# Optimization experiments

Hardware: AMD Instinct MI355X
Metric: run time of the kernel (lower is better)

The kernel has to match this reference:

```python
import jax, jax.numpy as jnp
import numpy as np
from jax import lax

K, E, HID, NH, L = 512, 256, 512, 8, 2
N, S1, S2, C, U, V, W = 2, 8, 9, 3, 8, 8, 8
S = S1 + S2 - 1  # 16, matches sum(cfg['seq_length']) - 1


def setup_inputs() -> dict:
    key = jax.random.key(0)
    ks = iter(jax.random.split(key, 40))
    g = lambda shape, s=0.02: jax.random.normal(next(ks), shape, jnp.float32) * s
    inp = {
        'code': jax.random.randint(next(ks), (N, S1, C, U, V, W), 0, K),
        'ncode': jax.random.randint(next(ks), (N, S2, C, U, V, W), 0, K),
        'emb': g((K, E)), 'pos_emb': g((S, E)),
        'Wq': g((L, 3, 3, 3, E, E)), 'bq': g((L, E)),
        'Wk': g((L, 3, 3, 3, E, E)), 'bk': g((L, E)),
        'Wv': g((L, 3, 3, 3, E, E)), 'bv': g((L, E)),
        'Wo': g((L, 3, 3, 3, E, E)), 'bo': g((L, E)),
        'ln1_g': jnp.ones((L, E)), 'ln1_b': jnp.zeros((L, E)),
        'ln2_g': jnp.ones((L, E)), 'ln2_b': jnp.zeros((L, E)),
        'Wc1': g((L, 3, 3, 3, E, HID)), 'bc1': g((L, HID)),
        'Wc2': g((L, 3, 3, 3, HID, E)), 'bc2': g((L, E)),
        'cls_W1': g((E, E)), 'cls_b1': jnp.zeros((E,)),
        'cls_ln_g': jnp.ones((E,)), 'cls_ln_b': jnp.zeros((E,)),
        'cls_W2': g((E, K)), 'cls_b2': jnp.zeros((K,)),
    }
    return inp


def _conv3d(t, w, b):
    # t: [B, S, U, V, W, Cin]; conv with kernel 3, stride 1, pad 1 (SAME)
    B_, S_, U_, V_, W_, Ci = t.shape
    y = lax.conv_general_dilated(t.reshape(B_ * S_, U_, V_, W_, Ci), w, (1, 1, 1), 'SAME',
                                 dimension_numbers=('NDHWC', 'DHWIO', 'NDHWC')) + b
    return y.reshape(B_, S_, U_, V_, W_, -1)


def _ln(t, g, b):
    mu = t.mean(-1, keepdims=True)
    var = ((t - mu) ** 2).mean(-1, keepdims=True)
    return (t - mu) * lax.rsqrt(var + 1e-5) * g + b


def _forward(code, ncode, emb, pos_emb, Wq, bq, Wk, bk, Wv, bv, Wo, bo,
             ln1_g, ln1_b, ln2_g, ln2_b, Wc1, bc1, Wc2, bc2,
             cls_W1, cls_b1, cls_ln_g, cls_ln_b, cls_W2, cls_b2):
    x = jnp.concatenate([code, ncode[:, :-1]], axis=1)  # [N, S, C, U, V, W]
    n, s, c, u, v, w = x.shape
    s2 = ncode.shape[1]
    x = x.transpose(0, 2, 1, 3, 4, 5).reshape(n * c, s, u, v, w)
    h = emb[x] + pos_emb[:s][None, :, None, None, None, :]  # [B, S, U, V, W, E]
    e = h.shape[-1]
    d = e // NH
    scale = jnp.asarray(d, h.dtype) ** 0.5
    # causal mask with first seq_length[0] columns fully visible
    m = jnp.tril(jnp.ones((s, s), bool)).at[:, :S1].set(True)

    def heads(t):
        return t.reshape(t.shape[0], s, u, v, w, NH, d).transpose(0, 5, 2, 3, 4, 1, 6)

    for i in range(Wq.shape[0]):
        q = heads(_conv3d(h, Wq[i], bq[i]))
        kk = heads(_conv3d(h, Wk[i], bk[i]))
        vv = heads(_conv3d(h, Wv[i], bv[i]))
        scores = jnp.einsum('bnuvwsd,bnuvwtd->bnuvwst', q, kk) / scale
        scores = jnp.where(m, scores, jnp.asarray(-1e30, scores.dtype))
        attn = jax.nn.softmax(scores, axis=-1)
        o = jnp.einsum('bnuvwst,bnuvwtd->bnuvwsd', attn, vv)
        o = o.transpose(0, 5, 2, 3, 4, 1, 6).reshape(h.shape[0], s, u, v, w, e)
        o = _conv3d(o, Wo[i], bo[i])
        h = _ln(h + o, ln1_g[i], ln1_b[i])
        f = _conv3d(jax.nn.gelu(_conv3d(h, Wc1[i], bc1[i]), approximate=False), Wc2[i], bc2[i])
        h = _ln(h + f, ln2_g[i], ln2_b[i])

    h = h[:, -s2:]
    h = h.reshape(n, c, s2, u, v, w, e).transpose(0, 2, 1, 3, 4, 5, 6)  # [N, S2, C, U, V, W, E]
    z = jnp.einsum('...e,ef->...f', h, cls_W1) + cls_b1
    z = jax.nn.gelu(_ln(z, cls_ln_g, cls_ln_b), approximate=False)
    z = jnp.einsum('...e,ek->...k', z, cls_W2) + cls_b2
    score = z.transpose(0, 6, 1, 2, 3, 4, 5)  # [N, K, S2, C, U, V, W]
    return score


def reference(code, ncode, emb, pos_emb, Wq, bq, Wk, bk, Wv, bv, Wo, bo,
              ln1_g, ln1_b, ln2_g, ln2_b, Wc1, bc1, Wc2, bc2,
              cls_W1, cls_b1, cls_ln_g, cls_ln_b, cls_W2, cls_b2):
    score = _forward(code, ncode, emb, pos_emb, Wq, bq, Wk, bk, Wv, bv, Wo, bo,
                     ln1_g, ln1_b, ln2_g, ln2_b, Wc1, bc1, Wc2, bc2,
                     cls_W1, cls_b1, cls_ln_g, cls_ln_b, cls_W2, cls_b2)
    logp = jax.nn.log_softmax(score, axis=1)
    nll = -jnp.take_along_axis(logp, ncode[:, None], axis=1)[:, 0]
    loss = nll.mean()
    pred = jnp.argmax(score, axis=1)
    return score, loss, pred
```

## Files before the change

### kernel.cpp

```cpp
#include <hip/hip_runtime.h>


typedef _Float16 f16;
typedef __attribute__((ext_vector_type(8))) _Float16 f16x8;
typedef __attribute__((ext_vector_type(4))) _Float16 f16x4;
typedef __attribute__((ext_vector_type(4))) float f32x4;

static constexpr long kSC = 14155776;
static constexpr float kDS = 4.8828125e-4f;

#define MFMA16(a, b, c) __builtin_amdgcn_mfma_f32_16x16x32_f16((a), (b), (c), 0, 0, 0)

__device__ __forceinline__ void gl16(const void* g, void* l) {
  __builtin_amdgcn_global_load_lds((const __attribute__((address_space(1))) void*)g,
                                   (__attribute__((address_space(3))) void*)l,
                                   16, 0, 0);
}

__device__ __forceinline__ float wave_sum_f(float x) {
#pragma unroll
  for (int m = 32; m; m >>= 1) x += __shfl_xor(x, m);
  return x;
}

__device__ __forceinline__ void split2(float x, f16* h, f16* l) {
  f16 hh = (f16)x;
  *h = hh;
  *l = (f16)((x - (float)hh) * 2048.0f);
}

__device__ __forceinline__ float rec2(f16 h, f16 l) {
  return (float)h + (float)l * kDS;
}

__device__ __forceinline__ float gelu_exact(float x) {
  return 0.5f * x * (1.0f + erff(x * 0.70710678118654752f));
}

__global__ __launch_bounds__(256) void wsplit_kernel(
    const float* __restrict__ src, f16* __restrict__ hi, f16* __restrict__ lo,
    int G, int Ci, int Co, int CoTot, int co0) {
  long n = (long)G * Ci * Co;
  long i = (long)blockIdx.x * 256 + threadIdx.x;
  if (i >= n) return;
  int co = (int)(i % Co);
  long t = i / Co;
  int ci = (int)(t % Ci);
  int g  = (int)(t / Ci);
  float x = src[i];
  long o = ((long)g * CoTot + co0 + co) * Ci + ci;
  split2(x, hi + o, lo + o);
}

__global__ __launch_bounds__(256) void bpack_kernel(
    const float* __restrict__ bq, const float* __restrict__ bk,
    const float* __restrict__ bv, float* __restrict__ dst) {
  int i = blockIdx.x * 256 + threadIdx.x;
  if (i < 256) dst[i] = bq[i];
  else if (i < 512) dst[i] = bk[i - 256];
  else if (i < 768) dst[i] = bv[i - 512];
}

__global__ __launch_bounds__(256) void embed_kernel(
    const int* __restrict__ code, const int* __restrict__ ncode,
    const float* __restrict__ emb, const float* __restrict__ pos,
    f16* __restrict__ Hh, f16* __restrict__ Hl) {
  int tok = blockIdx.x;
  int e = threadIdx.x;
  int g = tok >> 13;
  int rem = tok & 8191;
  int s = rem >> 9;
  int vox = rem & 511;
  int n = g / 3, c = g - 3 * n;
  int idx;
  if (s < 8) idx = code[((n * 8 + s) * 3 + c) * 512 + vox];
  else       idx = ncode[((n * 9 + (s - 8)) * 3 + c) * 512 + vox];
  float val = emb[idx * 256 + e] + pos[s * 256 + e];
  long o = (long)tok * 256 + e;
  split2(val, Hh + o, Hl + o);
}

template <int CIN, int COUTT, int ACT, int RESID>
__global__ __launch_bounds__(256, 2) void conv5_kernel(
    const f16* __restrict__ Xh, const f16* __restrict__ Xl, long xz_s, int xr,
    const f16* __restrict__ Wh, const f16* __restrict__ Wl,
    const float* __restrict__ bias,
    f16* __restrict__ Yh, f16* __restrict__ Yl, long yz_s, int yr, int nz) {
  constexpr int KB = CIN / 32;
  constexpr int NY = COUTT / 128;
  __shared__ __align__(16) f16 lsAll[32768];

  const int nwg = 64 * NY * nz;
  const int q = nwg >> 3;
  const int bid = blockIdx.x;
  const int wg = (bid & 7) * q + (bid >> 3);
  const int y = wg / (64 * nz);
  const int rem = wg - y * (64 * nz);
  const int z = rem >> 6;
  const int mt = rem & 63;
  const int img = mt >> 2, up = mt & 3;
  const int u0 = up * 2;
  const int coutb0 = y * 128;

  const int tid = threadIdx.x;
  const int wid = tid >> 6, lane = tid & 63;
  const int wm = wid >> 1, wn = wid & 1;
  const int l15 = lane & 15, lk = lane >> 4;

  const long xz = (long)z * xz_s;
  const long yz = (long)z * yz_s;

  f32x4 aA[4][4], aB[4][4];
#pragma unroll
  for (int mf = 0; mf < 4; ++mf)
#pragma unroll
    for (int nf = 0; nf < 4; ++nf) {
      float bv = bias[coutb0 + wn * 64 + nf * 16 + l15];
      aA[mf][nf] = (f32x4){bv, bv, bv, bv};
      aB[mf][nf] = (f32x4){0.f, 0.f, 0.f, 0.f};
    }

  const int swrow = tid >> 2;
  const int sslot = tid & 3;
  const int sswz = sslot ^ ((tid >> 3) & 3);

  auto stageA = [&](int kb) {
#pragma unroll
    for (int j = 0; j < 4; ++j) {
      const int uu = u0 - 1 + j;
      if (uu < 0 || uu >= 8) continue;
      const long g = xz + ((long)(img * 512 + uu * 64 + swrow)) * (long)xr
                     + kb * 32 + sswz * 8;
      gl16(Xh + g, &lsAll[j * 2048 + tid * 8]);
      gl16(Xl + g, &lsAll[8192 + j * 2048 + tid * 8]);
    }
  };
  auto stageB = [&](int o, int kb, int buf) {
#pragma unroll
    for (int i = 0; i < 2; ++i) {
      const long g = ((long)o * COUTT + coutb0 + i * 64 + swrow) * (long)CIN
                     + kb * 32 + sswz * 8;
      gl16(Wh + g, &lsAll[16384 + (buf * 2 + 0) * 4096 + i * 2048 + tid * 8]);
      gl16(Wl + g, &lsAll[16384 + (buf * 2 + 1) * 4096 + i * 2048 + tid * 8]);
    }
  };
  auto compute = [&](int o, int buf) {
    const int du = o / 9 - 1, dv = (o / 3) % 3 - 1, dw = o % 3 - 1;
    const int gu = u0 + wm + du;
    if ((unsigned)gu >= 8u) return;
    const int p = wm + 1 + du;
    f16x8 bh[4], bl[4];
#pragma unroll
    for (int nf = 0; nf < 4; ++nf) {
      const int rb = wn * 64 + nf * 16 + l15;
      const int sw = lk ^ ((rb >> 1) & 3);
      bh[nf] = *(const f16x8*)&lsAll[16384 + (buf * 2 + 0) * 4096 + rb * 32 + sw * 8];
      bl[nf] = *(const f16x8*)&lsAll[16384 + (buf * 2 + 1) * 4096 + rb * 32 + sw * 8];
    }
    __builtin_amdgcn_s_setprio(1);
#pragma unroll
    for (int mf = 0; mf < 4; ++mf) {
      const int vrow = mf * 16 + l15;
      const int vv = (vrow >> 3) + dv, ww = (vrow & 7) + dw;
      const bool ok = ((unsigned)vv < 8u) && ((unsigned)ww < 8u);
      f16x8 ah = {0, 0, 0, 0, 0, 0, 0, 0};
      f16x8 al = {0, 0, 0, 0, 0, 0, 0, 0};
      if (ok) {
        const int lrow = p * 64 + vv * 8 + ww;
        const int sw = lk ^ ((lrow >> 1) & 3);
        ah = *(const f16x8*)&lsAll[lrow * 32 + sw * 8];
        al = *(const f16x8*)&lsAll[8192 + lrow * 32 + sw * 8];
      }
#pragma unroll
      for (int nf = 0; nf < 4; ++nf) {
        aA[mf][nf] = MFMA16(ah, bh[nf], aA[mf][nf]);
        aB[mf][nf] = MFMA16(ah, bl[nf], aB[mf][nf]);
        aB[mf][nf] = MFMA16(al, bh[nf], aB[mf][nf]);
      }
    }
    __builtin_amdgcn_s_setprio(0);
  };

  stageA(0);
  stageB(0, 0, 0);
  __syncthreads();

#pragma unroll 1
  for (int kb = 0; kb < KB; ++kb) {
#pragma unroll 1
    for (int o = 0; o < 27; ++o) {
      const int cur = o & 1;
      if (o < 26) {
        stageB(o + 1, kb, cur ^ 1);
        asm volatile("s_waitcnt vmcnt(4)\n\ts_barrier" ::: "memory");
      } else {
        asm volatile("s_waitcnt vmcnt(0)\n\ts_barrier" ::: "memory");
      }
      compute(o, cur);
      asm volatile("s_barrier" ::: "memory");
    }
    if (kb + 1 < KB) {
      stageA(kb + 1);
      stageB(0, kb + 1, 0);
      asm volatile("s_waitcnt vmcnt(0)\n\ts_barrier" ::: "memory");
    }
  }

  float* sY = (float*)lsAll;
#pragma unroll 1
  for (int rh = 0; rh < 2; ++rh) {
    if (wm == rh) {
#pragma unroll
      for (int mf = 0; mf < 4; ++mf)
#pragma unroll
        for (int nf = 0; nf < 4; ++nf)
#pragma unroll
          for (int j = 0; j < 4; ++j) {
            const int row = mf * 16 + lk * 4 + j;
            const int col = wn * 64 + nf * 16 + l15;
            sY[row * 132 + col] = aA[mf][nf][j] + aB[mf][nf][j] * kDS;
          }
    }
    __syncthreads();
#pragma unroll
    for (int it = 0; it < 2; ++it) {
      const int row = it * 32 + (tid >> 3);
      const int c0 = (tid & 7) * 16;
      const long grow = (long)img * 512 + (u0 + rh) * 64 + row;
      const long gidx = yz + grow * (long)yr + coutb0 + c0;
      float yv[16];
#pragma unroll
      for (int i2 = 0; i2 < 16; ++i2) yv[i2] = sY[row * 132 + c0 + i2];
      if (ACT) {
#pragma unroll
        for (int i2 = 0; i2 < 16; ++i2) yv[i2] = gelu_exact(yv[i2]);
      }
      if (RESID) {
        f16x8 r0h = *(const f16x8*)&Yh[gidx];
        f16x8 r1h = *(const f16x8*)&Yh[gidx + 8];
        f16x8 r0l = *(const f16x8*)&Yl[gidx];
        f16x8 r1l = *(const f16x8*)&Yl[gidx + 8];
#pragma unroll
        for (int i2 = 0; i2 < 8; ++i2) {
          yv[i2] += rec2(r0h[i2], r0l[i2]);
          yv[8 + i2] += rec2(r1h[i2], r1l[i2]);
        }
      }
      f16x8 h0, h1, l0, l1;
#pragma unroll
      for (int i2 = 0; i2 < 8; ++i2) {
        f16 a, b;
        split2(yv[i2], &a, &b); h0[i2] = a; l0[i2] = b;
        split2(yv[8 + i2], &a, &b); h1[i2] = a; l1[i2] = b;
      }
      if (RESID) {
        *(f16x8*)&Yh[gidx] = h0;
        *(f16x8*)&Yh[gidx + 8] = h1;
        *(f16x8*)&Yl[gidx] = l0;
        *(f16x8*)&Yl[gidx + 8] = l1;
      } else {
        __builtin_nontemporal_store(h0, (f16x8*)&Yh[gidx]);
        __builtin_nontemporal_store(h1, (f16x8*)&Yh[gidx + 8]);
        __builtin_nontemporal_store(l0, (f16x8*)&Yl[gidx]);
        __builtin_nontemporal_store(l1, (f16x8*)&Yl[gidx + 8]);
      }
    }
    __syncthreads();
  }
}

template <int K_, int COUT, bool F32OUT>
__global__ __launch_bounds__(256) void gemm_kernel(
    const f16* __restrict__ Xh, const f16* __restrict__ Xl,
    const f16* __restrict__ Wh, const f16* __restrict__ Wl,
    const float* __restrict__ bias,
    f16* __restrict__ Yh, f16* __restrict__ Yl, float* __restrict__ Yf) {
  const int m0 = blockIdx.x * 64;
  const int coutb = blockIdx.y * 64;
  const int tid = threadIdx.x;
  const int wid = tid >> 6, lane = tid & 63;
  const int l15 = lane & 15, lk = lane >> 4;
  const int arow = m0 + wid * 16 + l15;

  f32x4 accA[4], accB[4];
#pragma unroll
  for (int cg = 0; cg < 4; ++cg) {
    float bv = bias[coutb + cg * 16 + l15];
    accA[cg] = (f32x4){bv, bv, bv, bv};
    accB[cg] = (f32x4){0.f, 0.f, 0.f, 0.f};
  }
  const f16* pah = Xh + (long)arow * K_ + lk * 8;
  const f16* pal = Xl + (long)arow * K_ + lk * 8;
  const f16* pbh = Wh + ((long)coutb + l15) * K_ + lk * 8;
  const f16* pbl = Wl + ((long)coutb + l15) * K_ + lk * 8;
#pragma unroll 2
  for (int kb = 0; kb < K_ / 32; ++kb) {
    f16x8 ah = *(const f16x8*)(pah + kb * 32);
    f16x8 al = *(const f16x8*)(pal + kb * 32);
#pragma unroll
    for (int cg = 0; cg < 4; ++cg) {
      f16x8 bh = *(const f16x8*)(pbh + (long)cg * 16 * K_ + kb * 32);
      f16x8 bl = *(const f16x8*)(pbl + (long)cg * 16 * K_ + kb * 32);
      accA[cg] = MFMA16(ah, bh, accA[cg]);
      accB[cg] = MFMA16(ah, bl, accB[cg]);
      accB[cg] = MFMA16(al, bh, accB[cg]);
    }
  }
  const long ybase = ((long)m0 + wid * 16) * (long)COUT + coutb;
#pragma unroll
  for (int cg = 0; cg < 4; ++cg)
#pragma unroll
    for (int j = 0; j < 4; ++j) {
      int r = lk * 4 + j;
      float y = accA[cg][j] + accB[cg][j] * kDS;
      long idx = ybase + (long)r * COUT + cg * 16 + l15;
      if (F32OUT) Yf[idx] = y;
      else        split2(y, Yh + idx, Yl + idx);
    }
}

__global__ __launch_bounds__(256) void attn_kernel(
    f16* __restrict__ QKVh, f16* __restrict__ QKVl) {
  __shared__ float sq[4][16][33];
  __shared__ float sk[4][16][33];
  __shared__ float sv[4][16][33];
  __shared__ float ss[4][16][17];
  const int wid = threadIdx.x >> 6, lane = threadIdx.x & 63;
  const int p = blockIdx.x * 4 + wid;
  const int cs = p >> 12;
  const int loc = p & 4095;
  const int nh = loc >> 9;
  const int vox = loc & 511;
  const int srow = lane >> 2;
  const int dp = (lane & 3) * 8;
  const long sbase = (long)cs * 6291456;
  const long base = sbase + ((long)(srow * 512 + vox)) * 768 + nh * 32 + dp;

  {
    f16x8 qh = *(const f16x8*)(QKVh + base);
    f16x8 ql = *(const f16x8*)(QKVl + base);
    f16x8 kh = *(const f16x8*)(QKVh + base + 256);
    f16x8 kl = *(const f16x8*)(QKVl + base + 256);
    f16x8 vh = *(const f16x8*)(QKVh + base + 512);
    f16x8 vl = *(const f16x8*)(QKVl + base + 512);
#pragma unroll
    for (int j = 0; j < 8; ++j) {
      sq[wid][srow][dp + j] = rec2(qh[j], ql[j]);
      sk[wid][srow][dp + j] = rec2(kh[j], kl[j]);
      sv[wid][srow][dp + j] = rec2(vh[j], vl[j]);
    }
  }
  __syncthreads();
#pragma unroll
  for (int pp = 0; pp < 4; ++pp) {
    int pr = lane * 4 + pp;
    int qi = pr >> 4, kt = pr & 15;
    float s = 0.f;
#pragma unroll
    for (int d = 0; d < 32; ++d) s += sq[wid][qi][d] * sk[wid][kt][d];
    bool allowed = (kt < 8) || (kt <= qi);
    ss[wid][qi][kt] = allowed ? s * 0.17677669529663687f : -1e30f;
  }
  __syncthreads();
  if (lane < 16) {
    float m = -1e30f;
#pragma unroll
    for (int t = 0; t < 16; ++t) m = fmaxf(m, ss[wid][lane][t]);
    float ex[16];
    float sum = 0.f;
#pragma unroll
    for (int t = 0; t < 16; ++t) { ex[t] = expf(ss[wid][lane][t] - m); sum += ex[t]; }
    float inv = 1.0f / sum;
#pragma unroll
    for (int t = 0; t < 16; ++t) ss[wid][lane][t] = ex[t] * inv;
  }
  __syncthreads();
  float o[8] = {0, 0, 0, 0, 0, 0, 0, 0};
#pragma unroll
  for (int t = 0; t < 16; ++t) {
    float a = ss[wid][srow][t];
#pragma unroll
    for (int j = 0; j < 8; ++j) o[j] += a * sv[wid][t][dp + j];
  }
#pragma unroll
  for (int j = 0; j < 8; ++j) split2(o[j], QKVh + base + j, QKVl + base + j);
}

__global__ __launch_bounds__(256) void ln_kernel(
    f16* __restrict__ Hh, f16* __restrict__ Hl,
    const float* __restrict__ gam, const float* __restrict__ bet) {
  const int wid = threadIdx.x >> 6, lane = threadIdx.x & 63;
  const long tok = (long)blockIdx.x * 4 + wid;
  const long base = tok * 256 + lane * 4;
  f16x4 hh = *(const f16x4*)(Hh + base);
  f16x4 hl = *(const f16x4*)(Hl + base);
  float v0 = rec2(hh[0], hl[0]), v1 = rec2(hh[1], hl[1]);
  float v2 = rec2(hh[2], hl[2]), v3 = rec2(hh[3], hl[3]);
  float mu = wave_sum_f(v0 + v1 + v2 + v3) * (1.0f / 256.0f);
  float d0 = v0 - mu, d1 = v1 - mu, d2 = v2 - mu, d3 = v3 - mu;
  float var = wave_sum_f(d0 * d0 + d1 * d1 + d2 * d2 + d3 * d3) * (1.0f / 256.0f);
  float rs = rsqrtf(var + 1e-5f);
  float4 gv = *(const float4*)(gam + lane * 4);
  float4 bv = *(const float4*)(bet + lane * 4);
  float y0 = d0 * rs * gv.x + bv.x, y1 = d1 * rs * gv.y + bv.y;
  float y2 = d2 * rs * gv.z + bv.z, y3 = d3 * rs * gv.w + bv.w;
  f16x4 oh, ol;
  f16 a, b2;
  split2(y0, &a, &b2); oh[0] = a; ol[0] = b2;
  split2(y1, &a, &b2); oh[1] = a; ol[1] = b2;
  split2(y2, &a, &b2); oh[2] = a; ol[2] = b2;
  split2(y3, &a, &b2); oh[3] = a; ol[3] = b2;
  *(f16x4*)(Hh + base) = oh;
  *(f16x4*)(Hl + base) = ol;
}

__global__ __launch_bounds__(256) void ln_gelu_kernel(
    f16* __restrict__ Zh, f16* __restrict__ Zl,
    const float* __restrict__ gam, const float* __restrict__ bet) {
  const int wid = threadIdx.x >> 6, lane = threadIdx.x & 63;
  const long tok = (long)blockIdx.x * 4 + wid;
  const long base = tok * 256 + lane * 4;
  f16x4 hh = *(const f16x4*)(Zh + base);
  f16x4 hl = *(const f16x4*)(Zl + base);
  float v0 = rec2(hh[0], hl[0]), v1 = rec2(hh[1], hl[1]);
  float v2 = rec2(hh[2], hl[2]), v3 = rec2(hh[3], hl[3]);
  float mu = wave_sum_f(v0 + v1 + v2 + v3) * (1.0f / 256.0f);
  float d0 = v0 - mu, d1 = v1 - mu, d2 = v2 - mu, d3 = v3 - mu;
  float var = wave_sum_f(d0 * d0 + d1 * d1 + d2 * d2 + d3 * d3) * (1.0f / 256.0f);
  float rs = rsqrtf(var + 1e-5f);
  float4 gv = *(const float4*)(gam + lane * 4);
  float4 bv = *(const float4*)(bet + lane * 4);
  float y0 = gelu_exact(d0 * rs * gv.x + bv.x);
  float y1 = gelu_exact(d1 * rs * gv.y + bv.y);
  float y2 = gelu_exact(d2 * rs * gv.z + bv.z);
  float y3 = gelu_exact(d3 * rs * gv.w + bv.w);
  f16x4 oh, ol;
  f16 a, b2;
  split2(y0, &a, &b2); oh[0] = a; ol[0] = b2;
  split2(y1, &a, &b2); oh[1] = a; ol[1] = b2;
  split2(y2, &a, &b2); oh[2] = a; ol[2] = b2;
  split2(y3, &a, &b2); oh[3] = a; ol[3] = b2;
  *(f16x4*)(Zh + base) = oh;
  *(f16x4*)(Zl + base) = ol;
}

__global__ __launch_bounds__(256) void gather_kernel(
    const f16* __restrict__ Hh, const f16* __restrict__ Hl, int n,
    f16* __restrict__ Xh, f16* __restrict__ Xl) {
  const int tc = blockIdx.x;
  const int e = threadIdx.x;
  const int s2 = tc / 1536;
  int r = tc - s2 * 1536;
  const int c = r >> 9;
  const int vox = r & 511;
  const int g = n * 3 + c;
  const int s = 7 + s2;
  const long src = ((long)(g * 16 + s) * 512 + vox) * 256 + e;
  const long dst = (long)tc * 256 + e;
  Xh[dst] = Hh[src];
  Xl[dst] = Hl[src];
}

__global__ __launch_bounds__(256) void transpose_kernel(
    const float* __restrict__ Z2, float* __restrict__ out) {
  __shared__ float tile[32][33];
  const int t0 = blockIdx.x * 32;
  const int k0 = blockIdx.y * 32;
  const int tx = threadIdx.x & 31;
  const int ty = threadIdx.x >> 5;
#pragma unroll
  for (int i = 0; i < 32; i += 8)
    tile[ty + i][tx] = Z2[((long)(t0 + ty + i)) * 512 + k0 + tx];
  __syncthreads();
#pragma unroll
  for (int i = 0; i < 32; i += 8)
    out[((long)(k0 + ty + i)) * 13824 + t0 + tx] = tile[tx][ty + i];
}

__global__ __launch_bounds__(256) void loss_pred_kernel(
    const float* __restrict__ Z2, const int* __restrict__ ncode,
    float* __restrict__ pred, float* __restrict__ partial) {
  __shared__ float sh[4];
  const int wid = threadIdx.x >> 6, lane = threadIdx.x & 63;
  const int tok = blockIdx.x * 4 + wid;
  const float* row = Z2 + (long)tok * 512;
  float4 a = *(const float4*)(row + lane * 8);
  float4 b = *(const float4*)(row + lane * 8 + 4);
  float vals[8] = {a.x, a.y, a.z, a.w, b.x, b.y, b.z, b.w};
  float mx = vals[0];
  int mi = lane * 8;
#pragma unroll
  for (int j = 1; j < 8; ++j)
    if (vals[j] > mx) { mx = vals[j]; mi = lane * 8 + j; }
#pragma unroll
  for (int m = 1; m < 64; m <<= 1) {
    float ox = __shfl_xor(mx, m);
    int oi = __shfl_xor(mi, m);
    if (ox > mx || (ox == mx && oi < mi)) { mx = ox; mi = oi; }
  }
  float se = 0.f;
#pragma unroll
  for (int j = 0; j < 8; ++j) se += expf(vals[j] - mx);
  se = wave_sum_f(se);
  if (lane == 0) {
    int tgt = ncode[tok];
    float nll = mx + logf(se) - row[tgt];
    pred[tok] = (float)mi;
    sh[wid] = nll;
  }
  __syncthreads();
  if (threadIdx.x == 0) partial[blockIdx.x] = sh[0] + sh[1] + sh[2] + sh[3];
}

__global__ __launch_bounds__(256) void loss_final_kernel(
    const float* __restrict__ partial, float* __restrict__ out) {
  __shared__ float sh[4];
  float s = 0.f;
  for (int i = threadIdx.x; i < 6912; i += 256) s += partial[i];
  s = wave_sum_f(s);
  if ((threadIdx.x & 63) == 0) sh[threadIdx.x >> 6] = s;
  __syncthreads();
  if (threadIdx.x == 0) out[0] = (sh[0] + sh[1] + sh[2] + sh[3]) * (1.0f / 27648.0f);
}

__global__ __launch_bounds__(256) void fill_kernel(float* __restrict__ p, long n, float v) {
  long i = (long)blockIdx.x * 256 + threadIdx.x;
  if (i < n) p[i] = v;
}

extern "C" void kernel_launch(void* const* d_in, const int* in_sizes, int n_in,
                              void* d_out, int out_size, void* d_ws, size_t ws_size,
                              hipStream_t stream) {
  const int* code   = (const int*)d_in[0];
  const int* ncode  = (const int*)d_in[1];
  const float* emb  = (const float*)d_in[2];
  const float* pos  = (const float*)d_in[3];
  const float* Wq   = (const float*)d_in[4];
  const float* bq   = (const float*)d_in[5];
  const float* Wk   = (const float*)d_in[6];
  const float* bk   = (const float*)d_in[7];
  const float* Wv   = (const float*)d_in[8];
  const float* bv   = (const float*)d_in[9];
  const float* Wo   = (const float*)d_in[10];
  const float* bo   = (const float*)d_in[11];
  const float* ln1g = (const float*)d_in[12];
  const float* ln1b = (const float*)d_in[13];
  const float* ln2g = (const float*)d_in[14];
  const float* ln2b = (const float*)d_in[15];
  const float* Wc1  = (const float*)d_in[16];
  const float* bc1  = (const float*)d_in[17];
  const float* Wc2  = (const float*)d_in[18];
  const float* bc2  = (const float*)d_in[19];
  const float* cW1  = (const float*)d_in[20];
  const float* cb1  = (const float*)d_in[21];
  const float* clng = (const float*)d_in[22];
  const float* clnb = (const float*)d_in[23];
  const float* cW2  = (const float*)d_in[24];
  const float* cb2  = (const float*)d_in[25];
  float* out = (float*)d_out;
  (void)in_sizes; (void)n_in; (void)out_size;

  const long WSLOT = 5308416;
  const long HSL   = 2097152;
  const long QSL   = 6291456;
  const long T1SL  = 4194304;
  const long CLMIN = 21233664;

  auto needf = [&](int ns) -> size_t {
    long slab = (long)ns * 2 * QSL;
    if (slab < CLMIN) slab = CLMIN;
    return (size_t)(2 * WSLOT + 2 * 12582912L + slab) * 2 + 6912 * 4 + 768 * 4 + 4096;
  };
  int NS = 0;
  if      (ws_size >= needf(6)) NS = 6;
  else if (ws_size >= needf(3)) NS = 3;
  else if (ws_size >= needf(2)) NS = 2;
  else if (ws_size >= needf(1)) NS = 1;
  if (NS == 0) {
    fill_kernel<<<dim3(109), 256, 0, stream>>>(out + kSC, 27649, -1.0f);
    return;
  }
  long slab_f16 = (long)NS * 2 * QSL;
  if (slab_f16 < CLMIN) slab_f16 = CLMIN;

  f16* wh = (f16*)d_ws;
  f16* wl = wh + WSLOT;
  f16* Hh = wl + WSLOT;
  f16* Hl = Hh + 12582912;
  f16* S  = Hl + 12582912;
  float* partial = (float*)(S + slab_f16);
  float* bcat = partial + 6912;

  const size_t WQKVO = 27u * 256 * 256;
  const size_t WC1SZ = 27u * 256 * 512;
  const size_t WC2SZ = 27u * 512 * 256;

  embed_kernel<<<dim3(49152), 256, 0, stream>>>(code, ncode, emb, pos, Hh, Hl);

  const int nchunk = 6 / NS;
  f16* qkvh = S;
  f16* qkvl = S + (long)NS * QSL;
  f16* t1h  = S;
  f16* t1l  = S + (long)NS * T1SL;

  for (int l = 0; l < 2; ++l) {
    const float* wq = Wq + (size_t)l * WQKVO;
    const float* wk = Wk + (size_t)l * WQKVO;
    const float* wv = Wv + (size_t)l * WQKVO;
    const float* wo = Wo + (size_t)l * WQKVO;
    const float* wc1 = Wc1 + (size_t)l * WC1SZ;
    const float* wc2 = Wc2 + (size_t)l * WC2SZ;
    bpack_kernel<<<dim3(3), 256, 0, stream>>>(bq + l * 256, bk + l * 256, bv + l * 256, bcat);
    for (int ch = 0; ch < nchunk; ++ch) {
      f16* Xh = Hh + (long)ch * NS * HSL;
      f16* Xl = Hl + (long)ch * NS * HSL;
      wsplit_kernel<<<dim3(6912), 256, 0, stream>>>(wq, wh, wl, 27, 256, 256, 768, 0);
      wsplit_kernel<<<dim3(6912), 256, 0, stream>>>(wk, wh, wl, 27, 256, 256, 768, 256);
      wsplit_kernel<<<dim3(6912), 256, 0, stream>>>(wv, wh, wl, 27, 256, 256, 768, 512);
      conv5_kernel<256, 768, 0, 0><<<dim3(64 * 6 * NS), 256, 0, stream>>>(
          Xh, Xl, HSL, 256, wh, wl, bcat, qkvh, qkvl, QSL, 768, NS);
      attn_kernel<<<dim3(NS * 1024), 256, 0, stream>>>(qkvh, qkvl);
      wsplit_kernel<<<dim3(6912), 256, 0, stream>>>(wo, wh, wl, 27, 256, 256, 256, 0);
      conv5_kernel<256, 256, 0, 1><<<dim3(64 * 2 * NS), 256, 0, stream>>>(
          qkvh, qkvl, QSL, 768, wh, wl, bo + l * 256, Xh, Xl, HSL, 256, NS);
      ln_kernel<<<dim3(2048 * NS), 256, 0, stream>>>(Xh, Xl, ln1g + l * 256, ln1b + l * 256);
      wsplit_kernel<<<dim3(13824), 256, 0, stream>>>(wc1, wh, wl, 27, 256, 512, 512, 0);
      conv5_kernel<256, 512, 1, 0><<<dim3(64 * 4 * NS), 256, 0, stream>>>(
          Xh, Xl, HSL, 256, wh, wl, bc1 + l * 512, t1h, t1l, T1SL, 512, NS);
      wsplit_kernel<<<dim3(13824), 256, 0, stream>>>(wc2, wh, wl, 27, 512, 256, 256, 0);
      conv5_kernel<512, 256, 0, 1><<<dim3(64 * 2 * NS), 256, 0, stream>>>(
          t1h, t1l, T1SL, 512, wh, wl, bc2 + l * 256, Xh, Xl, HSL, 256, NS);
      ln_kernel<<<dim3(2048 * NS), 256, 0, stream>>>(Xh, Xl, ln2g + l * 256, ln2b + l * 256);
    }
  }

  for (int n = 0; n < 2; ++n) {
    f16* Z1h = S;
    f16* Z1l = S + 3538944;
    f16* Xch = S + 7077888;
    f16* Xcl = S + 10616832;
    float* Z2 = (float*)(S + 7077888);
    gather_kernel<<<dim3(13824), 256, 0, stream>>>(Hh, Hl, n, Xch, Xcl);
    wsplit_kernel<<<dim3(256), 256, 0, stream>>>(cW1, wh, wl, 1, 256, 256, 256, 0);
    gemm_kernel<256, 256, false><<<dim3(216, 4), 256, 0, stream>>>(Xch, Xcl, wh, wl, cb1, Z1h, Z1l, nullptr);
    ln_gelu_kernel<<<dim3(3456), 256, 0, stream>>>(Z1h, Z1l, clng, clnb);
    wsplit_kernel<<<dim3(512), 256, 0, stream>>>(cW2, wh, wl, 1, 256, 512, 512, 0);
    gemm_kernel<256, 512, true><<<dim3(216, 8), 256, 0, stream>>>(Z1h, Z1l, wh, wl, cb2, nullptr, nullptr, Z2);
    transpose_kernel<<<dim3(432, 16), 256, 0, stream>>>(Z2, out + (long)n * 512 * 13824);
    loss_pred_kernel<<<dim3(3456), 256, 0, stream>>>(Z2, ncode + n * 13824,
                                                     out + kSC + 1 + n * 13824, partial + n * 3456);
  }
  loss_final_kernel<<<dim3(1), 256, 0, stream>>>(partial, out + kSC);
}
```

Before: 7.505 ms.

## Widen conv tiles to 256 output channels with 512 threads and triple-buffered weights

The implicit-GEMM 3D conv kernel now uses 512-thread workgroups (8 waves, 2x4) that each cover 256 output channels instead of 128, so each staged input tile is reused across twice as many output channels and fewer workgroups are launched. Weight staging becomes a three-slot ring that runs across the kb boundary: the next kb's first weight slice and its input slab are prefetched during the last tap rather than after a full drain. LDS use doubles to 128 KB per block and the epilogue is reworked to 4-wide stores, which lowers occupancy and raises register pressure under launch_bounds(512,2).

```diff
diff --git a/kernel.cpp b/kernel.cpp
--- a/kernel.cpp
+++ b/kernel.cpp
@@ -81,14 +81,14 @@
 }
 
 template <int CIN, int COUTT, int ACT, int RESID>
-__global__ __launch_bounds__(256, 2) void conv5_kernel(
+__global__ __launch_bounds__(512, 2) void conv6_kernel(
     const f16* __restrict__ Xh, const f16* __restrict__ Xl, long xz_s, int xr,
     const f16* __restrict__ Wh, const f16* __restrict__ Wl,
     const float* __restrict__ bias,
     f16* __restrict__ Yh, f16* __restrict__ Yl, long yz_s, int yr, int nz) {
   constexpr int KB = CIN / 32;
-  constexpr int NY = COUTT / 128;
-  __shared__ __align__(16) f16 lsAll[32768];
+  constexpr int NY = COUTT / 256;
+  __shared__ __align__(16) f16 lsAll[65536];
 
   const int nwg = 64 * NY * nz;
   const int q = nwg >> 3;
@@ -100,12 +100,13 @@
   const int mt = rem & 63;
   const int img = mt >> 2, up = mt & 3;
   const int u0 = up * 2;
-  const int coutb0 = y * 128;
+  const int coutb0 = y * 256;
 
   const int tid = threadIdx.x;
   const int wid = tid >> 6, lane = tid & 63;
-  const int wm = wid >> 1, wn = wid & 1;
+  const int wm = wid >> 2, wn = wid & 3;
   const int l15 = lane & 15, lk = lane >> 4;
+  const int sswz = (lane & 3) ^ ((lane >> 3) & 3);
 
   const long xz = (long)z * xz_s;
   const long yz = (long)z * yz_s;
@@ -120,28 +121,28 @@
       aB[mf][nf] = (f32x4){0.f, 0.f, 0.f, 0.f};
     }
 
-  const int swrow = tid >> 2;
-  const int sslot = tid & 3;
-  const int sswz = sslot ^ ((tid >> 3) & 3);
-
   auto stageA = [&](int kb) {
 #pragma unroll
-    for (int j = 0; j < 4; ++j) {
-      const int uu = u0 - 1 + j;
-      if (uu < 0 || uu >= 8) continue;
-      const long g = xz + ((long)(img * 512 + uu * 64 + swrow)) * (long)xr
-                     + kb * 32 + sswz * 8;
-      gl16(Xh + g, &lsAll[j * 2048 + tid * 8]);
-      gl16(Xl + g, &lsAll[8192 + j * 2048 + tid * 8]);
+    for (int r = 0; r < 2; ++r) {
+      const int arow = r * 128 + wid * 16 + (lane >> 2);
+      const int plane = (r * 128 + wid * 16) >> 6;
+      const int uu = u0 - 1 + plane;
+      if ((unsigned)uu >= 8u) continue;
+      const long gsrc = xz + ((long)(img * 512 + uu * 64 + (arow & 63))) * (long)xr
+                        + kb * 32 + sswz * 8;
+      gl16(Xh + gsrc, &lsAll[arow * 32 + (lane & 3) * 8]);
+      gl16(Xl + gsrc, &lsAll[8192 + arow * 32 + (lane & 3) * 8]);
     }
   };
   auto stageB = [&](int o, int kb, int buf) {
-#pragma unroll
-    for (int i = 0; i < 2; ++i) {
-      const long g = ((long)o * COUTT + coutb0 + i * 64 + swrow) * (long)CIN
-                     + kb * 32 + sswz * 8;
-      gl16(Wh + g, &lsAll[16384 + (buf * 2 + 0) * 4096 + i * 2048 + tid * 8]);
-      gl16(Wl + g, &lsAll[16384 + (buf * 2 + 1) * 4096 + i * 2048 + tid * 8]);
+    const int wb = 16384 + buf * 16384;
+#pragma unroll
+    for (int r = 0; r < 2; ++r) {
+      const int brow = r * 128 + wid * 16 + (lane >> 2);
+      const long gsrc = ((long)o * COUTT + coutb0 + brow) * (long)CIN
+                        + kb * 32 + sswz * 8;
+      gl16(Wh + gsrc, &lsAll[wb + brow * 32 + (lane & 3) * 8]);
+      gl16(Wl + gsrc, &lsAll[wb + 8192 + brow * 32 + (lane & 3) * 8]);
     }
   };
   auto compute = [&](int o, int buf) {
@@ -149,13 +150,14 @@
     const int gu = u0 + wm + du;
     if ((unsigned)gu >= 8u) return;
     const int p = wm + 1 + du;
+    const int wb = 16384 + buf * 16384;
     f16x8 bh[4], bl[4];
 #pragma unroll
     for (int nf = 0; nf < 4; ++nf) {
       const int rb = wn * 64 + nf * 16 + l15;
       const int sw = lk ^ ((rb >> 1) & 3);
-      bh[nf] = *(const f16x8*)&lsAll[16384 + (buf * 2 + 0) * 4096 + rb * 32 + sw * 8];
-      bl[nf] = *(const f16x8*)&lsAll[16384 + (buf * 2 + 1) * 4096 + rb * 32 + sw * 8];
+      bh[nf] = *(const f16x8*)&lsAll[wb + rb * 32 + sw * 8];
+      bl[nf] = *(const f16x8*)&lsAll[wb + 8192 + rb * 32 + sw * 8];
     }
     __builtin_amdgcn_s_setprio(1);
 #pragma unroll
@@ -183,28 +185,27 @@
 
   stageA(0);
   stageB(0, 0, 0);
-  __syncthreads();
+  asm volatile("s_waitcnt vmcnt(0)\n\ts_barrier" ::: "memory");
 
 #pragma unroll 1
   for (int kb = 0; kb < KB; ++kb) {
 #pragma unroll 1
     for (int o = 0; o < 27; ++o) {
-      const int cur = o & 1;
-      if (o < 26) {
-        stageB(o + 1, kb, cur ^ 1);
-        asm volatile("s_waitcnt vmcnt(4)\n\ts_barrier" ::: "memory");
-      } else {
-        asm volatile("s_waitcnt vmcnt(0)\n\ts_barrier" ::: "memory");
+      const int pph = kb * 27 + o;
+      const int bufc = pph % 3;
+      const bool last = (o == 26) && (kb + 1 == KB);
+      if (o < 26)           stageB(o + 1, kb, (pph + 1) % 3);
+      else if (kb + 1 < KB) stageB(0, kb + 1, (pph + 1) % 3);
+      if (last) asm volatile("s_waitcnt vmcnt(0)\n\ts_barrier" ::: "memory");
+      else      asm volatile("s_waitcnt vmcnt(4)\n\ts_barrier" ::: "memory");
+      compute(o, bufc);
+      if (o == 26 && kb + 1 < KB) {
+        asm volatile("s_barrier" ::: "memory");
+        stageA(kb + 1);
       }
-      compute(o, cur);
-      asm volatile("s_barrier" ::: "memory");
-    }
-    if (kb + 1 < KB) {
-      stageA(kb + 1);
-      stageB(0, kb + 1, 0);
-      asm volatile("s_waitcnt vmcnt(0)\n\ts_barrier" ::: "memory");
-    }
-  }
+    }
+  }
+  __syncthreads();
 
   float* sY = (float*)lsAll;
 #pragma unroll 1
@@ -218,51 +219,41 @@
           for (int j = 0; j < 4; ++j) {
             const int row = mf * 16 + lk * 4 + j;
             const int col = wn * 64 + nf * 16 + l15;
-            sY[row * 132 + col] = aA[mf][nf][j] + aB[mf][nf][j] * kDS;
+            sY[row * 260 + col] = aA[mf][nf][j] + aB[mf][nf][j] * kDS;
           }
     }
     __syncthreads();
+    const long growb = (long)img * 512 + (u0 + rh) * 64;
 #pragma unroll
     for (int it = 0; it < 2; ++it) {
-      const int row = it * 32 + (tid >> 3);
-      const int c0 = (tid & 7) * 16;
-      const long grow = (long)img * 512 + (u0 + rh) * 64 + row;
-      const long gidx = yz + grow * (long)yr + coutb0 + c0;
-      float yv[16];
-#pragma unroll
-      for (int i2 = 0; i2 < 16; ++i2) yv[i2] = sY[row * 132 + c0 + i2];
-      if (ACT) {
-#pragma unroll
-        for (int i2 = 0; i2 < 16; ++i2) yv[i2] = gelu_exact(yv[i2]);
-      }
-      if (RESID) {
-        f16x8 r0h = *(const f16x8*)&Yh[gidx];
-        f16x8 r1h = *(const f16x8*)&Yh[gidx + 8];
-        f16x8 r0l = *(const f16x8*)&Yl[gidx];
-        f16x8 r1l = *(const f16x8*)&Yl[gidx + 8];
-#pragma unroll
-        for (int i2 = 0; i2 < 8; ++i2) {
-          yv[i2] += rec2(r0h[i2], r0l[i2]);
-          yv[8 + i2] += rec2(r1h[i2], r1l[i2]);
+      const int row = it * 32 + (tid >> 4);
+#pragma unroll
+      for (int k = 0; k < 4; ++k) {
+        const int c0 = (tid & 15) * 4 + k * 64;
+        const long gidx = yz + (growb + row) * (long)yr + coutb0 + c0;
+        float yv[4];
+#pragma unroll
+        for (int i2 = 0; i2 < 4; ++i2) yv[i2] = sY[row * 260 + c0 + i2];
+        if (ACT) {
+#pragma unroll
+          for (int i2 = 0; i2 < 4; ++i2) yv[i2] = gelu_exact(yv[i2]);
         }
-      }
-      f16x8 h0, h1, l0, l1;
-#pragma unroll
-      for (int i2 = 0; i2 < 8; ++i2) {
-        f16 a, b;
-        split2(yv[i2], &a, &b); h0[i2] = a; l0[i2] = b;
-        split2(yv[8 + i2], &a, &b); h1[i2] = a; l1[i2] = b;
-      }
-      if (RESID) {
-        *(f16x8*)&Yh[gidx] = h0;
-        *(f16x8*)&Yh[gidx + 8] = h1;
-        *(f16x8*)&Yl[gidx] = l0;
-        *(f16x8*)&Yl[gidx + 8] = l1;
-      } else {
-        __builtin_nontemporal_store(h0, (f16x8*)&Yh[gidx]);
-        __builtin_nontemporal_store(h1, (f16x8*)&Yh[gidx + 8]);
-        __builtin_nontemporal_store(l0, (f16x8*)&Yl[gidx]);
-        __builtin_nontemporal_store(l1, (f16x8*)&Yl[gidx + 8]);
+        if (RESID) {
+          f16x4 rh_ = *(const f16x4*)&Yh[gidx];
+          f16x4 rl_ = *(const f16x4*)&Yl[gidx];
+#pragma unroll
+          for (int i2 = 0; i2 < 4; ++i2) yv[i2] += rec2(rh_[i2], rl_[i2]);
+        }
+        f16x4 hv, lv;
+#pragma unroll
+        for (int i2 = 0; i2 < 4; ++i2) { f16 a, b; split2(yv[i2], &a, &b); hv[i2] = a; lv[i2] = b; }
+        if (RESID) {
+          *(f16x4*)&Yh[gidx] = hv;
+          *(f16x4*)&Yl[gidx] = lv;
+        } else {
+          __builtin_nontemporal_store(hv, (f16x4*)&Yh[gidx]);
+          __builtin_nontemporal_store(lv, (f16x4*)&Yl[gidx]);
+        }
       }
     }
     __syncthreads();
@@ -617,18 +608,18 @@
       wsplit_kernel<<<dim3(6912), 256, 0, stream>>>(wq, wh, wl, 27, 256, 256, 768, 0);
       wsplit_kernel<<<dim3(6912), 256, 0, stream>>>(wk, wh, wl, 27, 256, 256, 768, 256);
       wsplit_kernel<<<dim3(6912), 256, 0, stream>>>(wv, wh, wl, 27, 256, 256, 768, 512);
-      conv5_kernel<256, 768, 0, 0><<<dim3(64 * 6 * NS), 256, 0, stream>>>(
+      conv6_kernel<256, 768, 0, 0><<<dim3(64 * 3 * NS), 512, 0, stream>>>(
           Xh, Xl, HSL, 256, wh, wl, bcat, qkvh, qkvl, QSL, 768, NS);
       attn_kernel<<<dim3(NS * 1024), 256, 0, stream>>>(qkvh, qkvl);
       wsplit_kernel<<<dim3(6912), 256, 0, stream>>>(wo, wh, wl, 27, 256, 256, 256, 0);
-      conv5_kernel<256, 256, 0, 1><<<dim3(64 * 2 * NS), 256, 0, stream>>>(
+      conv6_kernel<256, 256, 0, 1><<<dim3(64 * 1 * NS), 512, 0, stream>>>(
           qkvh, qkvl, QSL, 768, wh, wl, bo + l * 256, Xh, Xl, HSL, 256, NS);
       ln_kernel<<<dim3(2048 * NS), 256, 0, stream>>>(Xh, Xl, ln1g + l * 256, ln1b + l * 256);
       wsplit_kernel<<<dim3(13824), 256, 0, stream>>>(wc1, wh, wl, 27, 256, 512, 512, 0);
-      conv5_kernel<256, 512, 1, 0><<<dim3(64 * 4 * NS), 256, 0, stream>>>(
+      conv6_kernel<256, 512, 1, 0><<<dim3(64 * 2 * NS), 512, 0, stream>>>(
           Xh, Xl, HSL, 256, wh, wl, bc1 + l * 512, t1h, t1l, T1SL, 512, NS);
       wsplit_kernel<<<dim3(13824), 256, 0, stream>>>(wc2, wh, wl, 27, 512, 256, 256, 0);
-      conv5_kernel<512, 256, 0, 1><<<dim3(64 * 2 * NS), 256, 0, stream>>>(
+      conv6_kernel<512, 256, 0, 1><<<dim3(64 * 1 * NS), 512, 0, stream>>>(
           t1h, t1l, T1SL, 512, wh, wl, bc2 + l * 256, Xh, Xl, HSL, 256, NS);
       ln_kernel<<<dim3(2048 * NS), 256, 0, stream>>>(Xh, Xl, ln2g + l * 256, ln2b + l * 256);
     }
```

New measurement: 8.493 ms. +13.2%, slower.

## Triple-buffer conv weight tiles and overlap stages across channel blocks

Applied to the files above, without the earlier changes.

The conv kernel's weight staging goes from double to triple buffering, which removes the second barrier after each tap's compute. The first weight tile of the next input-channel block is prefetched during the last tap, and the activation tile reload is issued right after the final compute of a block, instead of a separate fully synchronised reload phase. This is meant to cut barrier stalls and load-latency bubbles at tap and block boundaries. In exchange, LDS use per block rises from 64 KB to 80 KB, which may limit co-residency of two blocks per CU.

```diff
diff --git a/kernel.cpp b/kernel.cpp
--- a/kernel.cpp
+++ b/kernel.cpp
@@ -81,14 +81,14 @@
 }
 
 template <int CIN, int COUTT, int ACT, int RESID>
-__global__ __launch_bounds__(256, 2) void conv5_kernel(
+__global__ __launch_bounds__(256, 2) void conv8_kernel(
     const f16* __restrict__ Xh, const f16* __restrict__ Xl, long xz_s, int xr,
     const f16* __restrict__ Wh, const f16* __restrict__ Wl,
     const float* __restrict__ bias,
     f16* __restrict__ Yh, f16* __restrict__ Yl, long yz_s, int yr, int nz) {
   constexpr int KB = CIN / 32;
   constexpr int NY = COUTT / 128;
-  __shared__ __align__(16) f16 lsAll[32768];
+  __shared__ __align__(16) f16 lsAll[40960];
 
   const int nwg = 64 * NY * nz;
   const int q = nwg >> 3;
@@ -121,8 +121,7 @@
     }
 
   const int swrow = tid >> 2;
-  const int sslot = tid & 3;
-  const int sswz = sslot ^ ((tid >> 3) & 3);
+  const int sswz = (tid & 3) ^ ((tid >> 3) & 3);
 
   auto stageA = [&](int kb) {
 #pragma unroll
@@ -136,12 +135,13 @@
     }
   };
   auto stageB = [&](int o, int kb, int buf) {
+    const int wb = 16384 + buf * 8192;
 #pragma unroll
     for (int i = 0; i < 2; ++i) {
       const long g = ((long)o * COUTT + coutb0 + i * 64 + swrow) * (long)CIN
                      + kb * 32 + sswz * 8;
-      gl16(Wh + g, &lsAll[16384 + (buf * 2 + 0) * 4096 + i * 2048 + tid * 8]);
-      gl16(Wl + g, &lsAll[16384 + (buf * 2 + 1) * 4096 + i * 2048 + tid * 8]);
+      gl16(Wh + g, &lsAll[wb + i * 2048 + tid * 8]);
+      gl16(Wl + g, &lsAll[wb + 4096 + i * 2048 + tid * 8]);
     }
   };
   auto compute = [&](int o, int buf) {
@@ -149,13 +149,14 @@
     const int gu = u0 + wm + du;
     if ((unsigned)gu >= 8u) return;
     const int p = wm + 1 + du;
+    const int wb = 16384 + buf * 8192;
     f16x8 bh[4], bl[4];
 #pragma unroll
     for (int nf = 0; nf < 4; ++nf) {
       const int rb = wn * 64 + nf * 16 + l15;
       const int sw = lk ^ ((rb >> 1) & 3);
-      bh[nf] = *(const f16x8*)&lsAll[16384 + (buf * 2 + 0) * 4096 + rb * 32 + sw * 8];
-      bl[nf] = *(const f16x8*)&lsAll[16384 + (buf * 2 + 1) * 4096 + rb * 32 + sw * 8];
+      bh[nf] = *(const f16x8*)&lsAll[wb + rb * 32 + sw * 8];
+      bl[nf] = *(const f16x8*)&lsAll[wb + 4096 + rb * 32 + sw * 8];
     }
     __builtin_amdgcn_s_setprio(1);
 #pragma unroll
@@ -183,28 +184,27 @@
 
   stageA(0);
   stageB(0, 0, 0);
-  __syncthreads();
-
+
+  int bcur = 0;
 #pragma unroll 1
   for (int kb = 0; kb < KB; ++kb) {
 #pragma unroll 1
     for (int o = 0; o < 27; ++o) {
-      const int cur = o & 1;
-      if (o < 26) {
-        stageB(o + 1, kb, cur ^ 1);
-        asm volatile("s_waitcnt vmcnt(4)\n\ts_barrier" ::: "memory");
-      } else {
-        asm volatile("s_waitcnt vmcnt(0)\n\ts_barrier" ::: "memory");
+      int bnext = bcur + 1; if (bnext == 3) bnext = 0;
+      const bool haveNext = !(o == 26 && kb + 1 == KB);
+      if (o < 26)           stageB(o + 1, kb, bnext);
+      else if (kb + 1 < KB) stageB(0, kb + 1, bnext);
+      if (haveNext) asm volatile("s_waitcnt vmcnt(4)\n\ts_barrier" ::: "memory");
+      else          asm volatile("s_waitcnt vmcnt(0)\n\ts_barrier" ::: "memory");
+      compute(o, bcur);
+      if (o == 26 && kb + 1 < KB) {
+        asm volatile("s_barrier" ::: "memory");
+        stageA(kb + 1);
       }
-      compute(o, cur);
-      asm volatile("s_barrier" ::: "memory");
-    }
-    if (kb + 1 < KB) {
-      stageA(kb + 1);
-      stageB(0, kb + 1, 0);
-      asm volatile("s_waitcnt vmcnt(0)\n\ts_barrier" ::: "memory");
-    }
-  }
+      bcur = bnext;
+    }
+  }
+  __syncthreads();
 
   float* sY = (float*)lsAll;
 #pragma unroll 1
@@ -617,18 +617,18 @@
       wsplit_kernel<<<dim3(6912), 256, 0, stream>>>(wq, wh, wl, 27, 256, 256, 768, 0);
       wsplit_kernel<<<dim3(6912), 256, 0, stream>>>(wk, wh, wl, 27, 256, 256, 768, 256);
       wsplit_kernel<<<dim3(6912), 256, 0, stream>>>(wv, wh, wl, 27, 256, 256, 768, 512);
-      conv5_kernel<256, 768, 0, 0><<<dim3(64 * 6 * NS), 256, 0, stream>>>(
+      conv8_kernel<256, 768, 0, 0><<<dim3(64 * 6 * NS), 256, 0, stream>>>(
           Xh, Xl, HSL, 256, wh, wl, bcat, qkvh, qkvl, QSL, 768, NS);
       attn_kernel<<<dim3(NS * 1024), 256, 0, stream>>>(qkvh, qkvl);
       wsplit_kernel<<<dim3(6912), 256, 0, stream>>>(wo, wh, wl, 27, 256, 256, 256, 0);
-      conv5_kernel<256, 256, 0, 1><<<dim3(64 * 2 * NS), 256, 0, stream>>>(
+      conv8_kernel<256, 256, 0, 1><<<dim3(64 * 2 * NS), 256, 0, stream>>>(
           qkvh, qkvl, QSL, 768, wh, wl, bo + l * 256, Xh, Xl, HSL, 256, NS);
       ln_kernel<<<dim3(2048 * NS), 256, 0, stream>>>(Xh, Xl, ln1g + l * 256, ln1b + l * 256);
       wsplit_kernel<<<dim3(13824), 256, 0, stream>>>(wc1, wh, wl, 27, 256, 512, 512, 0);
-      conv5_kernel<256, 512, 1, 0><<<dim3(64 * 4 * NS), 256, 0, stream>>>(
+      conv8_kernel<256, 512, 1, 0><<<dim3(64 * 4 * NS), 256, 0, stream>>>(
           Xh, Xl, HSL, 256, wh, wl, bc1 + l * 512, t1h, t1l, T1SL, 512, NS);
       wsplit_kernel<<<dim3(13824), 256, 0, stream>>>(wc2, wh, wl, 27, 512, 256, 256, 0);
-      conv5_kernel<512, 256, 0, 1><<<dim3(64 * 2 * NS), 256, 0, stream>>>(
+      conv8_kernel<512, 256, 0, 1><<<dim3(64 * 2 * NS), 256, 0, stream>>>(
           t1h, t1l, T1SL, 512, wh, wl, bc2 + l * 256, Xh, Xl, HSL, 256, NS);
       ln_kernel<<<dim3(2048 * NS), 256, 0, stream>>>(Xh, Xl, ln2g + l * 256, ln2b + l * 256);
     }
```

After: 7.604 ms. No clear change (+1.3%).
